# Optimization experiments

Hardware: AMD Instinct MI355X
Metric: run time of the kernel (lower is better)

Reference implementation:

```python
import jax, jax.numpy as jnp
import numpy as np

N_NODES = 100000
N_EDGES = 1600000
HIDDEN = 128


def setup_inputs() -> dict:
    key = jax.random.key(0)
    k1, k2, k3, k4, k5 = jax.random.split(key, 5)
    probabilities = jax.random.uniform(k1, (N_EDGES,), dtype=jnp.float32)
    hidden = jax.random.normal(k2, (N_NODES, HIDDEN), dtype=jnp.float32)
    edge_index = jax.random.randint(k3, (2, N_EDGES), 0, N_NODES, dtype=jnp.int32)
    # nn.Linear(hidden_dim, hidden_dim): weight [out, in], bias [out]
    bound = 1.0 / np.sqrt(HIDDEN)
    lin_w = jax.random.uniform(k4, (HIDDEN, HIDDEN), minval=-bound, maxval=bound, dtype=jnp.float32)
    lin_b = jax.random.uniform(k5, (HIDDEN,), minval=-bound, maxval=bound, dtype=jnp.float32)
    return {"probabilities": probabilities, "hidden": hidden, "edge_index": edge_index,
            "lin_w": lin_w, "lin_b": lin_b}


def reference(probabilities, hidden, edge_index, lin_w, lin_b):
    # gather target-node hidden states: [E, H]
    target_hidden = hidden[edge_index[1]]
    # scale each message by its edge probability
    weighted_msg = target_hidden * probabilities[:, None]
    # scatter_add into source-node buckets: [N, H]
    aggregated = jax.ops.segment_sum(weighted_msg, edge_index[0], num_segments=hidden.shape[0])
    # trailing linear: y = aggregated @ W^T + b
    return aggregated @ lin_w.T + lin_b
```

## Files before the change

### kernel.cpp

```cpp
#include <hip/hip_runtime.h>

#define HIDDEN 128
#define NPB 64
#define CHUNK 4096
#define NBMAX 2048
#define CAP 1280

typedef __attribute__((ext_vector_type(8))) short bf16x8;
typedef __attribute__((ext_vector_type(4))) float f32x4;

static __device__ __forceinline__ ushort f2bf(float f) {
    uint u = __float_as_uint(f);
    uint r = (u + 0x7fffu + ((u >> 16) & 1u)) >> 16;
    return (ushort)r;
}

static __device__ __forceinline__ void splitt(float f, ushort& h, ushort& l) {
    uint u = __float_as_uint(f);
    h = (ushort)(u >> 16);
    l = f2bf(f - __uint_as_float(u & 0xffff0000u));
}

static __device__ __forceinline__ bf16x8 mkfrag(ushort4 a, ushort4 b) {
    bf16x8 f;
    f[0] = (short)a.x; f[1] = (short)a.y; f[2] = (short)a.z; f[3] = (short)a.w;
    f[4] = (short)b.x; f[5] = (short)b.y; f[6] = (short)b.z; f[7] = (short)b.w;
    return f;
}

__global__ __launch_bounds__(256, 2) void bg_k(
    const int* __restrict__ ei, const float* __restrict__ prob,
    const float* __restrict__ A, const float* __restrict__ W,
    int* __restrict__ gcur, int2* __restrict__ ed, ushort* __restrict__ hp,
    int E, int N, int NB, int BINB, int GEMB)
{
    __shared__ char smem[65536];
    const int t = threadIdx.x;

    if ((int)blockIdx.x < BINB) {
        int* hist = (int*)smem;
        int* base = (int*)(smem + 4 * NBMAX);
        const int e0 = blockIdx.x * CHUNK;

        for (int i = t; i < NB; i += 256) hist[i] = 0;
        __syncthreads();

        int  bs[16];
        int2 pl[16];
        #pragma unroll
        for (int j = 0; j < 16; ++j) {
            int e = e0 + j * 256 + t;
            if (e < E) {
                int src = ei[e];
                int tgt = ei[E + e];
                int p15 = min((int)(prob[e] * 32768.0f + 0.5f), 32767);
                int b   = src >> 6;
                bs[j] = b;
                pl[j] = make_int2(tgt, ((src & (NPB - 1)) << 15) | p15);
                atomicAdd(&hist[b], 1);
            } else bs[j] = -1;
        }
        __syncthreads();

        for (int i = t; i < NB; i += 256) {
            int c = hist[i];
            base[i] = c ? (i * CAP + atomicAdd(&gcur[i], c)) : 0;
            hist[i] = 0;
        }
        __syncthreads();

        #pragma unroll
        for (int j = 0; j < 16; ++j) {
            if (bs[j] >= 0) {
                int r = atomicAdd(&hist[bs[j]], 1);
                ed[base[bs[j]] + r] = pl[j];
            }
        }
        __syncthreads();
    }

    if ((int)blockIdx.x >= GEMB) return;
    ushort* a_hi = (ushort*)smem;
    ushort* a_lo = (ushort*)(smem + 32768);

    const int n0 = blockIdx.x * 128;

    #pragma unroll
    for (int i = 0; i < 16; ++i) {
        int idx4 = t + 256 * i;
        int row  = idx4 >> 5;
        int kq   = idx4 & 31;
        int n    = n0 + row;
        float4 v = (n < N) ? ((const float4*)A)[(size_t)n * 32 + kq]
                           : make_float4(0.f, 0.f, 0.f, 0.f);
        ushort4 h, l;
        splitt(v.x, h.x, l.x);
        splitt(v.y, h.y, l.y);
        splitt(v.z, h.z, l.z);
        splitt(v.w, h.w, l.w);
        uint off = (uint)((row << 8) + (kq << 3)) ^ (uint)((row & 7) << 4);
        *(ushort4*)((char*)a_hi + off) = h;
        *(ushort4*)((char*)a_lo + off) = l;
    }

    const int w  = t >> 6;
    const int l  = t & 63;
    const int wr = w >> 1;
    const int wc = w & 1;
    const int lg = l >> 4;
    const int li = l & 15;

    bf16x8 wfh[4][4], wfl[4][4];
    #pragma unroll
    for (int c = 0; c < 4; ++c) {
        int o = wc * 64 + c * 16 + li;
        #pragma unroll
        for (int ks = 0; ks < 4; ++ks) {
            int kb = ks * 32 + lg * 4;
            const float* pw = W + o * 128 + kb;
            float4 w0 = *(const float4*)(pw);
            float4 w1 = *(const float4*)(pw + 16);
            ushort4 h0, l0, h1, l1;
            splitt(w0.x, h0.x, l0.x); splitt(w0.y, h0.y, l0.y);
            splitt(w0.z, h0.z, l0.z); splitt(w0.w, h0.w, l0.w);
            splitt(w1.x, h1.x, l1.x); splitt(w1.y, h1.y, l1.y);
            splitt(w1.z, h1.z, l1.z); splitt(w1.w, h1.w, l1.w);
            wfh[c][ks] = mkfrag(h0, h1);
            wfl[c][ks] = mkfrag(l0, l1);
        }
    }

    f32x4 acc[4][4];
    #pragma unroll
    for (int m = 0; m < 4; ++m)
        #pragma unroll
        for (int c = 0; c < 4; ++c)
            acc[m][c] = (f32x4){0.f, 0.f, 0.f, 0.f};

    __syncthreads();

    #pragma unroll
    for (int ks = 0; ks < 4; ++ks) {
        int kb2 = (ks * 32 + lg * 4) * 2;
        #pragma unroll
        for (int m = 0; m < 4; ++m) {
            int row  = wr * 64 + m * 16 + li;
            uint bse = (uint)(row << 8);
            uint swz = (uint)((row & 7) << 4);
            uint o0  = (bse + kb2) ^ swz;
            uint o1  = (bse + kb2 + 32) ^ swz;
            ushort4 h0 = *(ushort4*)((char*)a_hi + o0);
            ushort4 h1 = *(ushort4*)((char*)a_hi + o1);
            ushort4 q0 = *(ushort4*)((char*)a_lo + o0);
            ushort4 q1 = *(ushort4*)((char*)a_lo + o1);
            bf16x8 ah = mkfrag(h0, h1);
            bf16x8 al = mkfrag(q0, q1);
            #pragma unroll
            for (int c = 0; c < 4; ++c) {
                acc[m][c] = __builtin_amdgcn_mfma_f32_16x16x32_bf16(ah, wfh[c][ks], acc[m][c], 0, 0, 0);
                acc[m][c] = __builtin_amdgcn_mfma_f32_16x16x32_bf16(ah, wfl[c][ks], acc[m][c], 0, 0, 0);
                acc[m][c] = __builtin_amdgcn_mfma_f32_16x16x32_bf16(al, wfh[c][ks], acc[m][c], 0, 0, 0);
            }
        }
    }

    #pragma unroll
    for (int m = 0; m < 4; ++m) {
        #pragma unroll
        for (int i = 0; i < 4; ++i) {
            int n = n0 + wr * 64 + m * 16 + lg * 4 + i;
            if (n < N) {
                ushort* dst = hp + (size_t)n * 128 + wc * 64 + li;
                #pragma unroll
                for (int c = 0; c < 4; ++c)
                    dst[c * 16] = f2bf(acc[m][c][i]);
            }
        }
    }
}

__global__ __launch_bounds__(256, 8) void agg_k(
    const int*  __restrict__ gcur,
    const int2* __restrict__ ed,
    const ushort* __restrict__ hp,
    const float* __restrict__ bias,
    float*       __restrict__ out,
    int N)
{
    __shared__ int2 buf[CAP];
    __shared__ int  hist[NPB];
    __shared__ int  hoff[NPB + 1];

    const int t   = threadIdx.x;
    const int b   = blockIdx.x;
    const int nb0 = b * NPB;
    const int beg = b * CAP;
    const int c   = min(gcur[b], CAP);

    if (t < NPB) hist[t] = 0;
    __syncthreads();

    for (int i = t; i < c; i += 256)
        atomicAdd(&hist[(ed[beg + i].y >> 15) & (NPB - 1)], 1);
    __syncthreads();

    if (t < NPB) {
        int x = hist[t];
        int v = x;
        #pragma unroll
        for (int d = 1; d < 64; d <<= 1) {
            int u = __shfl_up(v, d);
            if (t >= d) v += u;
        }
        hoff[t] = v - x;
        hist[t] = 0;
        if (t == NPB - 1) hoff[NPB] = v;
    }
    __syncthreads();

    for (int i = t; i < c; i += 256) {
        int2 e = ed[beg + i];
        int lo = (e.y >> 15) & (NPB - 1);
        int r  = atomicAdd(&hist[lo], 1);
        buf[hoff[lo] + r] = e;
    }
    __syncthreads();

    const int wv = t >> 6;
    const int l  = t & 63;
    const int eg = l >> 4;
    const int cs = l & 15;
    const uint4* hpq = (const uint4*)hp;
    const float ps = 1.0f / 32768.0f;
    const float2 bv = ((const float2*)bias)[cs * 4 + eg];

    for (int ln = wv; ln < NPB; ln += 4) {
        int n = nb0 + ln;
        if (n >= N) break;
        const int s = hoff[ln];
        const int e = hoff[ln + 1];

        float acc[8];
        #pragma unroll
        for (int k = 0; k < 8; ++k) acc[k] = 0.f;

        int i = s;
        for (; i + 16 <= e; i += 16) {
            int2 d0 = buf[i + eg];
            int2 d1 = buf[i + 4 + eg];
            int2 d2 = buf[i + 8 + eg];
            int2 d3 = buf[i + 12 + eg];
            uint4 q0 = hpq[(size_t)d0.x * 16 + cs];
            uint4 q1 = hpq[(size_t)d1.x * 16 + cs];
            uint4 q2 = hpq[(size_t)d2.x * 16 + cs];
            uint4 q3 = hpq[(size_t)d3.x * 16 + cs];
            float p0 = (float)(d0.y & 0x7fff) * ps;
            float p1 = (float)(d1.y & 0x7fff) * ps;
            float p2 = (float)(d2.y & 0x7fff) * ps;
            float p3 = (float)(d3.y & 0x7fff) * ps;
            uint u;
            u = q0.x; acc[0] += p0 * __uint_as_float(u << 16); acc[1] += p0 * __uint_as_float(u & 0xffff0000u);
            u = q0.y; acc[2] += p0 * __uint_as_float(u << 16); acc[3] += p0 * __uint_as_float(u & 0xffff0000u);
            u = q0.z; acc[4] += p0 * __uint_as_float(u << 16); acc[5] += p0 * __uint_as_float(u & 0xffff0000u);
            u = q0.w; acc[6] += p0 * __uint_as_float(u << 16); acc[7] += p0 * __uint_as_float(u & 0xffff0000u);
            u = q1.x; acc[0] += p1 * __uint_as_float(u << 16); acc[1] += p1 * __uint_as_float(u & 0xffff0000u);
            u = q1.y; acc[2] += p1 * __uint_as_float(u << 16); acc[3] += p1 * __uint_as_float(u & 0xffff0000u);
            u = q1.z; acc[4] += p1 * __uint_as_float(u << 16); acc[5] += p1 * __uint_as_float(u & 0xffff0000u);
            u = q1.w; acc[6] += p1 * __uint_as_float(u << 16); acc[7] += p1 * __uint_as_float(u & 0xffff0000u);
            u = q2.x; acc[0] += p2 * __uint_as_float(u << 16); acc[1] += p2 * __uint_as_float(u & 0xffff0000u);
            u = q2.y; acc[2] += p2 * __uint_as_float(u << 16); acc[3] += p2 * __uint_as_float(u & 0xffff0000u);
            u = q2.z; acc[4] += p2 * __uint_as_float(u << 16); acc[5] += p2 * __uint_as_float(u & 0xffff0000u);
            u = q2.w; acc[6] += p2 * __uint_as_float(u << 16); acc[7] += p2 * __uint_as_float(u & 0xffff0000u);
            u = q3.x; acc[0] += p3 * __uint_as_float(u << 16); acc[1] += p3 * __uint_as_float(u & 0xffff0000u);
            u = q3.y; acc[2] += p3 * __uint_as_float(u << 16); acc[3] += p3 * __uint_as_float(u & 0xffff0000u);
            u = q3.z; acc[4] += p3 * __uint_as_float(u << 16); acc[5] += p3 * __uint_as_float(u & 0xffff0000u);
            u = q3.w; acc[6] += p3 * __uint_as_float(u << 16); acc[7] += p3 * __uint_as_float(u & 0xffff0000u);
        }
        for (; i + 8 <= e; i += 8) {
            int2 d0 = buf[i + eg];
            int2 d1 = buf[i + 4 + eg];
            uint4 q0 = hpq[(size_t)d0.x * 16 + cs];
            uint4 q1 = hpq[(size_t)d1.x * 16 + cs];
            float p0 = (float)(d0.y & 0x7fff) * ps;
            float p1 = (float)(d1.y & 0x7fff) * ps;
            uint u;
            u = q0.x; acc[0] += p0 * __uint_as_float(u << 16); acc[1] += p0 * __uint_as_float(u & 0xffff0000u);
            u = q0.y; acc[2] += p0 * __uint_as_float(u << 16); acc[3] += p0 * __uint_as_float(u & 0xffff0000u);
            u = q0.z; acc[4] += p0 * __uint_as_float(u << 16); acc[5] += p0 * __uint_as_float(u & 0xffff0000u);
            u = q0.w; acc[6] += p0 * __uint_as_float(u << 16); acc[7] += p0 * __uint_as_float(u & 0xffff0000u);
            u = q1.x; acc[0] += p1 * __uint_as_float(u << 16); acc[1] += p1 * __uint_as_float(u & 0xffff0000u);
            u = q1.y; acc[2] += p1 * __uint_as_float(u << 16); acc[3] += p1 * __uint_as_float(u & 0xffff0000u);
            u = q1.z; acc[4] += p1 * __uint_as_float(u << 16); acc[5] += p1 * __uint_as_float(u & 0xffff0000u);
            u = q1.w; acc[6] += p1 * __uint_as_float(u << 16); acc[7] += p1 * __uint_as_float(u & 0xffff0000u);
        }
        for (; i < e; i += 4) {
            int ei_ = i + eg;
            int2 d = (ei_ < e) ? buf[ei_] : make_int2(0, 0);
            uint4 q = hpq[(size_t)d.x * 16 + cs];
            float p = (float)(d.y & 0x7fff) * ps;
            uint u;
            u = q.x; acc[0] += p * __uint_as_float(u << 16); acc[1] += p * __uint_as_float(u & 0xffff0000u);
            u = q.y; acc[2] += p * __uint_as_float(u << 16); acc[3] += p * __uint_as_float(u & 0xffff0000u);
            u = q.z; acc[4] += p * __uint_as_float(u << 16); acc[5] += p * __uint_as_float(u & 0xffff0000u);
            u = q.w; acc[6] += p * __uint_as_float(u << 16); acc[7] += p * __uint_as_float(u & 0xffff0000u);
        }

        #pragma unroll
        for (int k = 0; k < 8; ++k) {
            float vv = acc[k];
            vv += __shfl_xor(vv, 16);
            vv += __shfl_xor(vv, 32);
            acc[k] = vv;
        }

        float2 r;
        r.x = acc[eg * 2]     + bv.x;
        r.y = acc[eg * 2 + 1] + bv.y;
        ((float2*)(out + (size_t)n * HIDDEN))[cs * 4 + eg] = r;
    }
}

extern "C" void kernel_launch(void* const* d_in, const int* in_sizes, int n_in,
                              void* d_out, int out_size, void* d_ws, size_t ws_size,
                              hipStream_t stream)
{
    const float* prob   = (const float*)d_in[0];
    const float* hidden = (const float*)d_in[1];
    const int*   ei     = (const int*)  d_in[2];
    const float* W      = (const float*)d_in[3];
    const float* bias   = (const float*)d_in[4];
    float*       out    = (float*)d_out;

    const int E    = in_sizes[0];
    const int N    = in_sizes[1] / HIDDEN;
    const int NB   = (N + NPB - 1) / NPB;
    const int BINB = (E + CHUNK - 1) / CHUNK;
    const int GEMB = (N + 127) / 128;
    const int GRID = (BINB > GEMB) ? BINB : GEMB;

    char* w = (char*)d_ws;
    int* gcur = (int*)w;
    size_t ib = ((size_t)NB * 4 + 255) & ~(size_t)255;
    int2*   ed = (int2*)(w + ib);
    ushort* hp = (ushort*)(w + ib + (size_t)NB * CAP * 8);

    (void)hipMemsetAsync(gcur, 0, (size_t)NB * sizeof(int), stream);

    bg_k<<<GRID, 256, 0, stream>>>(ei, prob, hidden, W, gcur, ed, hp,
                                   E, N, NB, BINB, GEMB);
    agg_k<<<NB, 256, 0, stream>>>(gcur, ed, hp, bias, out, N);
}
```

Before: 246.2 us.

## Split binning and GEMM into separate blocks, halve LDS, stage K in two halves

Binning and GEMM work now go to separate blocks in one grid of BINB+GEMB blocks, where they used to share blocks. The GEMM stages the A tile in two K-halves, which halves shared memory to 32KB and raises launch bounds to 4 blocks per SM. The point is higher occupancy and better overlap of the memory-bound binning with the GEMM. Separately, the 16-edge unrolled loop in the aggregation kernel is removed, which lowers register pressure but gives up some memory-level parallelism. The two-phase staging adds an extra barrier per block.

```diff
diff --git a/kernel.cpp b/kernel.cpp
--- a/kernel.cpp
+++ b/kernel.cpp
@@ -28,13 +28,13 @@
     return f;
 }
 
-__global__ __launch_bounds__(256, 2) void bg_k(
+__global__ __launch_bounds__(256, 4) void bg_k(
     const int* __restrict__ ei, const float* __restrict__ prob,
     const float* __restrict__ A, const float* __restrict__ W,
     int* __restrict__ gcur, int2* __restrict__ ed, ushort* __restrict__ hp,
-    int E, int N, int NB, int BINB, int GEMB)
+    int E, int N, int NB, int BINB)
 {
-    __shared__ char smem[65536];
+    __shared__ __align__(16) char smem[32768];
     const int t = threadIdx.x;
 
     if ((int)blockIdx.x < BINB) {
@@ -76,33 +76,13 @@
                 ed[base[bs[j]] + r] = pl[j];
             }
         }
-        __syncthreads();
-    }
-
-    if ((int)blockIdx.x >= GEMB) return;
+        return;
+    }
+
     ushort* a_hi = (ushort*)smem;
-    ushort* a_lo = (ushort*)(smem + 32768);
-
-    const int n0 = blockIdx.x * 128;
-
-    #pragma unroll
-    for (int i = 0; i < 16; ++i) {
-        int idx4 = t + 256 * i;
-        int row  = idx4 >> 5;
-        int kq   = idx4 & 31;
-        int n    = n0 + row;
-        float4 v = (n < N) ? ((const float4*)A)[(size_t)n * 32 + kq]
-                           : make_float4(0.f, 0.f, 0.f, 0.f);
-        ushort4 h, l;
-        splitt(v.x, h.x, l.x);
-        splitt(v.y, h.y, l.y);
-        splitt(v.z, h.z, l.z);
-        splitt(v.w, h.w, l.w);
-        uint off = (uint)((row << 8) + (kq << 3)) ^ (uint)((row & 7) << 4);
-        *(ushort4*)((char*)a_hi + off) = h;
-        *(ushort4*)((char*)a_lo + off) = l;
-    }
-
+    ushort* a_lo = (ushort*)(smem + 16384);
+
+    const int n0 = ((int)blockIdx.x - BINB) * 128;
     const int w  = t >> 6;
     const int l  = t & 63;
     const int wr = w >> 1;
@@ -137,31 +117,53 @@
         for (int c = 0; c < 4; ++c)
             acc[m][c] = (f32x4){0.f, 0.f, 0.f, 0.f};
 
-    __syncthreads();
-
     #pragma unroll
-    for (int ks = 0; ks < 4; ++ks) {
-        int kb2 = (ks * 32 + lg * 4) * 2;
-        #pragma unroll
-        for (int m = 0; m < 4; ++m) {
-            int row  = wr * 64 + m * 16 + li;
-            uint bse = (uint)(row << 8);
-            uint swz = (uint)((row & 7) << 4);
-            uint o0  = (bse + kb2) ^ swz;
-            uint o1  = (bse + kb2 + 32) ^ swz;
-            ushort4 h0 = *(ushort4*)((char*)a_hi + o0);
-            ushort4 h1 = *(ushort4*)((char*)a_hi + o1);
-            ushort4 q0 = *(ushort4*)((char*)a_lo + o0);
-            ushort4 q1 = *(ushort4*)((char*)a_lo + o1);
-            bf16x8 ah = mkfrag(h0, h1);
-            bf16x8 al = mkfrag(q0, q1);
+    for (int h = 0; h < 2; ++h) {
+        #pragma unroll
+        for (int i = 0; i < 8; ++i) {
+            int idx4 = t + 256 * i;
+            int row  = idx4 >> 4;
+            int kq   = idx4 & 15;
+            int n    = n0 + row;
+            float4 v = (n < N) ? ((const float4*)A)[(size_t)n * 32 + h * 16 + kq]
+                               : make_float4(0.f, 0.f, 0.f, 0.f);
+            ushort4 hh, ll;
+            splitt(v.x, hh.x, ll.x);
+            splitt(v.y, hh.y, ll.y);
+            splitt(v.z, hh.z, ll.z);
+            splitt(v.w, hh.w, ll.w);
+            uint off = (uint)((row << 7) + (kq << 3)) ^ (uint)((row & 7) << 4);
+            *(ushort4*)((char*)a_hi + off) = hh;
+            *(ushort4*)((char*)a_lo + off) = ll;
+        }
+        __syncthreads();
+
+        #pragma unroll
+        for (int ks = 0; ks < 2; ++ks) {
+            int kb2 = (ks * 32 + lg * 4) * 2;
             #pragma unroll
-            for (int c = 0; c < 4; ++c) {
-                acc[m][c] = __builtin_amdgcn_mfma_f32_16x16x32_bf16(ah, wfh[c][ks], acc[m][c], 0, 0, 0);
-                acc[m][c] = __builtin_amdgcn_mfma_f32_16x16x32_bf16(ah, wfl[c][ks], acc[m][c], 0, 0, 0);
-                acc[m][c] = __builtin_amdgcn_mfma_f32_16x16x32_bf16(al, wfh[c][ks], acc[m][c], 0, 0, 0);
+            for (int m = 0; m < 4; ++m) {
+                int row  = wr * 64 + m * 16 + li;
+                uint bse = (uint)(row << 7);
+                uint swz = (uint)((row & 7) << 4);
+                uint o0  = (bse + kb2) ^ swz;
+                uint o1  = (bse + kb2 + 32) ^ swz;
+                ushort4 h0 = *(ushort4*)((char*)a_hi + o0);
+                ushort4 h1 = *(ushort4*)((char*)a_hi + o1);
+                ushort4 q0 = *(ushort4*)((char*)a_lo + o0);
+                ushort4 q1 = *(ushort4*)((char*)a_lo + o1);
+                bf16x8 ah = mkfrag(h0, h1);
+                bf16x8 al = mkfrag(q0, q1);
+                int kg = h * 2 + ks;
+                #pragma unroll
+                for (int c = 0; c < 4; ++c) {
+                    acc[m][c] = __builtin_amdgcn_mfma_f32_16x16x32_bf16(ah, wfh[c][kg], acc[m][c], 0, 0, 0);
+                    acc[m][c] = __builtin_amdgcn_mfma_f32_16x16x32_bf16(ah, wfl[c][kg], acc[m][c], 0, 0, 0);
+                    acc[m][c] = __builtin_amdgcn_mfma_f32_16x16x32_bf16(al, wfh[c][kg], acc[m][c], 0, 0, 0);
+                }
             }
         }
+        if (h == 0) __syncthreads();
     }
 
     #pragma unroll
@@ -245,37 +247,6 @@
         for (int k = 0; k < 8; ++k) acc[k] = 0.f;
 
         int i = s;
-        for (; i + 16 <= e; i += 16) {
-            int2 d0 = buf[i + eg];
-            int2 d1 = buf[i + 4 + eg];
-            int2 d2 = buf[i + 8 + eg];
-            int2 d3 = buf[i + 12 + eg];
-            uint4 q0 = hpq[(size_t)d0.x * 16 + cs];
-            uint4 q1 = hpq[(size_t)d1.x * 16 + cs];
-            uint4 q2 = hpq[(size_t)d2.x * 16 + cs];
-            uint4 q3 = hpq[(size_t)d3.x * 16 + cs];
-            float p0 = (float)(d0.y & 0x7fff) * ps;
-            float p1 = (float)(d1.y & 0x7fff) * ps;
-            float p2 = (float)(d2.y & 0x7fff) * ps;
-            float p3 = (float)(d3.y & 0x7fff) * ps;
-            uint u;
-            u = q0.x; acc[0] += p0 * __uint_as_float(u << 16); acc[1] += p0 * __uint_as_float(u & 0xffff0000u);
-            u = q0.y; acc[2] += p0 * __uint_as_float(u << 16); acc[3] += p0 * __uint_as_float(u & 0xffff0000u);
-            u = q0.z; acc[4] += p0 * __uint_as_float(u << 16); acc[5] += p0 * __uint_as_float(u & 0xffff0000u);
-            u = q0.w; acc[6] += p0 * __uint_as_float(u << 16); acc[7] += p0 * __uint_as_float(u & 0xffff0000u);
-            u = q1.x; acc[0] += p1 * __uint_as_float(u << 16); acc[1] += p1 * __uint_as_float(u & 0xffff0000u);
-            u = q1.y; acc[2] += p1 * __uint_as_float(u << 16); acc[3] += p1 * __uint_as_float(u & 0xffff0000u);
-            u = q1.z; acc[4] += p1 * __uint_as_float(u << 16); acc[5] += p1 * __uint_as_float(u & 0xffff0000u);
-            u = q1.w; acc[6] += p1 * __uint_as_float(u << 16); acc[7] += p1 * __uint_as_float(u & 0xffff0000u);
-            u = q2.x; acc[0] += p2 * __uint_as_float(u << 16); acc[1] += p2 * __uint_as_float(u & 0xffff0000u);
-            u = q2.y; acc[2] += p2 * __uint_as_float(u << 16); acc[3] += p2 * __uint_as_float(u & 0xffff0000u);
-            u = q2.z; acc[4] += p2 * __uint_as_float(u << 16); acc[5] += p2 * __uint_as_float(u & 0xffff0000u);
-            u = q2.w; acc[6] += p2 * __uint_as_float(u << 16); acc[7] += p2 * __uint_as_float(u & 0xffff0000u);
-            u = q3.x; acc[0] += p3 * __uint_as_float(u << 16); acc[1] += p3 * __uint_as_float(u & 0xffff0000u);
-            u = q3.y; acc[2] += p3 * __uint_as_float(u << 16); acc[3] += p3 * __uint_as_float(u & 0xffff0000u);
-            u = q3.z; acc[4] += p3 * __uint_as_float(u << 16); acc[5] += p3 * __uint_as_float(u & 0xffff0000u);
-            u = q3.w; acc[6] += p3 * __uint_as_float(u << 16); acc[7] += p3 * __uint_as_float(u & 0xffff0000u);
-        }
         for (; i + 8 <= e; i += 8) {
             int2 d0 = buf[i + eg];
             int2 d1 = buf[i + 4 + eg];
@@ -336,7 +307,6 @@
     const int NB   = (N + NPB - 1) / NPB;
     const int BINB = (E + CHUNK - 1) / CHUNK;
     const int GEMB = (N + 127) / 128;
-    const int GRID = (BINB > GEMB) ? BINB : GEMB;
 
     char* w = (char*)d_ws;
     int* gcur = (int*)w;
@@ -346,7 +316,7 @@
 
     (void)hipMemsetAsync(gcur, 0, (size_t)NB * sizeof(int), stream);
 
-    bg_k<<<GRID, 256, 0, stream>>>(ei, prob, hidden, W, gcur, ed, hp,
-                                   E, N, NB, BINB, GEMB);
+    bg_k<<<BINB + GEMB, 256, 0, stream>>>(ei, prob, hidden, W, gcur, ed, hp,
+                                          E, N, NB, BINB);
     agg_k<<<NB, 256, 0, stream>>>(gcur, ed, hp, bias, out, N);
 }
```

Result: slower. 290.2 us (+17.9%).
